# Optimization experiments

Hardware: AMD Instinct MI355X
Metric: run time of the kernel (lower is better)

## Reference

```python
import jax, jax.numpy as jnp
import numpy as np

OUT, IN = 11008, 4096  # LLaMA-7B FFN up-projection


def _unpack(packed, shape):
    """Unpack 2-bit fields (4 ternary values per byte, stored as q+1 in {0,1,2})."""
    shifts = jnp.arange(4, dtype=packed.dtype) * 2
    vals = (packed[:, None] >> shifts) & 3            # [n_bytes, 4]
    n = shape[0] * shape[1]
    q = vals.reshape(-1)[:n].astype(jnp.float32) - 1.0  # back to {-1,0,1}
    return q.reshape(shape)


def _pack(q):
    """Pack ternary int values {-1,0,1} -> 2-bit fields, 4 per byte."""
    flat = (q + 1).reshape(-1)
    pad = (-flat.shape[0]) % 4
    flat = jnp.pad(flat, (0, pad))
    groups = flat.reshape(-1, 4)
    weights = (jnp.int32(1) << (jnp.arange(4, dtype=jnp.int32) * 2))
    return jnp.sum(groups * weights, axis=1).astype(jnp.int32)


def setup_inputs() -> dict:
    key = jax.random.key(0)
    kx, kw = jax.random.split(key)
    x = jax.random.normal(kx, (4, 2048, IN), dtype=jnp.float32)
    # build a realistic weight, then absmean-quantize it (per output row)
    W = jax.random.normal(kw, (OUT, IN), dtype=jnp.float32) * 0.02
    weight_scale = jnp.mean(jnp.abs(W), axis=1, keepdims=True)  # [OUT, 1]
    q = jnp.clip(jnp.round(W / weight_scale), -1.0, 1.0).astype(jnp.int32)
    packed_weight = _pack(q)  # [OUT*IN/4] int32 bytes
    return {"x": x, "packed_weight": packed_weight, "weight_scale": weight_scale}


def reference(x, packed_weight, weight_scale):
    # unpack ternary weights, dequantize via per-row scale, dense GEMM
    W = _unpack(packed_weight, (OUT, IN)) * weight_scale  # [OUT, IN] fp32
    return jnp.einsum('bsi,oi->bso', x, W)
```

## Files before the change

kernel.cpp:

```cpp
#include <hip/hip_runtime.h>
#include <hip/hip_bf16.h>


#define M_DIM 8192
#define N_DIM 11008
#define K_DIM 4096
#define BM 128
#define BN 256
#define BK 64
#define KT 64
#define NB_N 43
#define NWG 2752

#define XBF_BYTES ((size_t)M_DIM * K_DIM * 2)
#define BT_BYTES  ((size_t)N_DIM * K_DIM / 4)
#define WS_NEED   (XBF_BYTES + BT_BYTES)

typedef __attribute__((ext_vector_type(8))) short bf16x8;
typedef __attribute__((ext_vector_type(4))) float f32x4;

__device__ inline unsigned int bf16b(float f) {
  union { __hip_bfloat16 h; unsigned short u; } cv;
  cv.h = __float2bfloat16(f);
  return (unsigned int)cv.u;
}

__device__ __forceinline__ void gload_lds16(const void* g, void* l) {
  __builtin_amdgcn_global_load_lds(
      (const __attribute__((address_space(1))) unsigned int*)g,
      (__attribute__((address_space(3))) unsigned int*)l, 16, 0, 0);
}

#define XCVT_BLOCKS 16384
#define PACK_BLOCKS 5504
__global__ __launch_bounds__(256)
void xcvt_kernel(const float* __restrict__ X, unsigned short* __restrict__ Xbf) {
  const size_t i8 = ((size_t)blockIdx.x * 256 + threadIdx.x) * 8;
  float4 a = *(const float4*)(X + i8);
  float4 c = *(const float4*)(X + i8 + 4);
  uint4 o;
  o.x = bf16b(a.x) | (bf16b(a.y) << 16);
  o.y = bf16b(a.z) | (bf16b(a.w) << 16);
  o.z = bf16b(c.x) | (bf16b(c.y) << 16);
  o.w = bf16b(c.z) | (bf16b(c.w) << 16);
  *(uint4*)(Xbf + i8) = o;
}

__global__ __launch_bounds__(256)
void btight_kernel(const int* __restrict__ PW, unsigned char* __restrict__ Bt) {
  const size_t i8 = ((size_t)blockIdx.x * 256 + threadIdx.x) * 8;
  int4 p = *(const int4*)(PW + i8);
  int4 q = *(const int4*)(PW + i8 + 4);
  uint2 o;
  o.x = (unsigned)(p.x & 255) | ((unsigned)(p.y & 255) << 8) |
        ((unsigned)(p.z & 255) << 16) | ((unsigned)(p.w & 255) << 24);
  o.y = (unsigned)(q.x & 255) | ((unsigned)(q.y & 255) << 8) |
        ((unsigned)(q.z & 255) << 16) | ((unsigned)(q.w & 255) << 24);
  *(uint2*)(Bt + i8) = o;
}

__global__ __launch_bounds__(256, 2)
void qlin_p4_kernel(const unsigned short* __restrict__ Xbf,
                    const unsigned char* __restrict__ Bt,
                    const float* __restrict__ SC, float* __restrict__ OUT) {
  __shared__ unsigned short As[3][BM * BK];
  __shared__ unsigned char  Bs[3][BN * 16];

  const int tid = threadIdx.x;
  const int lane = tid & 63;
  const int w = tid >> 6;

  const int wg = blockIdx.x;
  const int swz = (wg & 7) * (NWG / 8) + (wg >> 3);
  const int bm = swz / NB_N;
  const int bn = swz - bm * NB_N;

  const int l3 = lane >> 3;
  const char* ab0 = (const char*)Xbf +
      (size_t)(bm * BM + w * 32 + l3) * (K_DIM * 2) + ((lane & 7) ^ l3) * 16;
  const char* bb = (const char*)Bt + (size_t)(bn * BN + w * 64 + lane) * (K_DIM / 4);

#define STAGE(IDX, KT_) do {                                           \
    unsigned short* ad_ = &As[IDX][w * 2048];                          \
    unsigned char* bd_ = &Bs[IDX][w * 1024];                           \
    gload_lds16(ab0 + (KT_)*128,           ad_);                       \
    gload_lds16(ab0 + (KT_)*128 + 65536,   ad_ + 512);                 \
    gload_lds16(ab0 + (KT_)*128 + 131072,  ad_ + 1024);                \
    gload_lds16(ab0 + (KT_)*128 + 196608,  ad_ + 1536);                \
    gload_lds16(bb  + (KT_)*16,            bd_);                       \
  } while (0)

  f32x4 acc[8][4];
#pragma unroll
  for (int i = 0; i < 8; ++i)
#pragma unroll
    for (int j = 0; j < 4; ++j) acc[i][j] = (f32x4){0.f, 0.f, 0.f, 0.f};

  const int l4 = lane >> 4;
  const int axor = lane & 7;
  const int arow = (lane & 15) * 128;
  const int hb = l4 >> 1;
  const unsigned hoff = (unsigned)(l4 & 1) * 16;
  const int rbase = (w * 64 + (lane & 15)) * 16 + hb * 4;

  bf16x8 af[4];
  bf16x8 bfr[4];
  unsigned d4[4];

#define DSA(CB, KK, H) do {                                                    \
    const char* asb_ = (const char*)&As[CB][0];                                \
    _Pragma("unroll")                                                          \
    for (int m = 0; m < 4; ++m)                                                \
      af[m] = *(const bf16x8*)(asb_ + ((H) * 4 + m) * 2048 + arow +            \
                               ((((KK) * 4 + l4) ^ axor) << 4));               \
  } while (0)

#define DSB(CB, KK) do {                                                       \
    const unsigned char* bsb_ = &Bs[CB][0];                                    \
    _Pragma("unroll")                                                          \
    for (int n = 0; n < 4; ++n)                                                \
      d4[n] = *(const unsigned*)(bsb_ + rbase + n * 256 + (KK) * 8);           \
  } while (0)

#define UNPACK() do {                                                          \
    _Pragma("unroll")                                                          \
    for (int n = 0; n < 4; ++n) {                                              \
      const unsigned w16 = (d4[n] >> hoff) & 0xFFFFu;                          \
      const unsigned u = w16 | (w16 << 14);                                    \
      union { uint4 s; bf16x8 v; } t;                                          \
      t.s.x = ((u << 14) & 0xC000C000u) + 0x40004000u;                         \
      t.s.y = ((u << 10) & 0xC000C000u) + 0x40004000u;                         \
      t.s.z = ((u << 6)  & 0xC000C000u) + 0x40004000u;                         \
      t.s.w = ((u << 2)  & 0xC000C000u) + 0x40004000u;                         \
      bfr[n] = t.v;                                                            \
    }                                                                          \
  } while (0)

#define MFMA16(H) do {                                                         \
    _Pragma("unroll")                                                          \
    for (int m = 0; m < 4; ++m)                                                \
      _Pragma("unroll")                                                        \
      for (int n = 0; n < 4; ++n)                                              \
        acc[(H) * 4 + m][n] = __builtin_amdgcn_mfma_f32_16x16x32_bf16(         \
            af[m], bfr[n], acc[(H) * 4 + m][n], 0, 0, 0);                      \
  } while (0)

#define BAR() __builtin_amdgcn_s_barrier()
#define LGKM0() asm volatile("s_waitcnt lgkmcnt(0)" ::: "memory")
#define PRIO(P) __builtin_amdgcn_s_setprio(P)

  STAGE(0, 0);
  STAGE(1, 1);
  asm volatile("s_waitcnt vmcnt(5)" ::: "memory");
  BAR();

  int cb = 0, sb = 2;
  for (int kt = 0; kt < KT; ++kt) {
    const bool more = (kt + 2 < KT);
    DSA(cb, 0, 0);
    DSB(cb, 0);
    if (more) STAGE(sb, kt + 2);
    BAR(); LGKM0(); PRIO(1);
    UNPACK();
    MFMA16(0);
    PRIO(0); BAR();
    DSA(cb, 0, 1);
    BAR(); LGKM0(); PRIO(1);
    MFMA16(1);
    PRIO(0); BAR();
    DSA(cb, 1, 0);
    DSB(cb, 1);
    BAR(); LGKM0(); PRIO(1);
    UNPACK();
    MFMA16(0);
    PRIO(0); BAR();
    DSA(cb, 1, 1);
    if (more) { asm volatile("s_waitcnt vmcnt(5)" ::: "memory"); }
    else      { asm volatile("s_waitcnt vmcnt(0)" ::: "memory"); }
    BAR(); LGKM0(); PRIO(1);
    MFMA16(1);
    PRIO(0); BAR();
    cb = (cb == 2) ? 0 : cb + 1;
    sb = (sb == 2) ? 0 : sb + 1;
  }
#undef STAGE
#undef DSA
#undef DSB
#undef UNPACK
#undef MFMA16

  const int gc0 = bn * BN + w * 64 + (lane & 15);
  const int gr0 = bm * BM + (l4 << 2);
  float sc[4];
#pragma unroll
  for (int n = 0; n < 4; ++n) sc[n] = -0.5f * SC[gc0 + n * 16];
#pragma unroll
  for (int m = 0; m < 8; ++m)
#pragma unroll
    for (int n = 0; n < 4; ++n)
#pragma unroll
      for (int r = 0; r < 4; ++r)
        OUT[(size_t)(gr0 + m * 16 + r) * N_DIM + gc0 + n * 16] = acc[m][n][r] * sc[n];
}

#define BSTRIDE 20
__global__ __launch_bounds__(256, 2)
void qlin_fused_kernel(const float* __restrict__ X, const int* __restrict__ PW,
                       const float* __restrict__ SC, float* __restrict__ OUT) {
  __shared__ unsigned short Asf[128 * 64];
  __shared__ unsigned char Bp[256 * BSTRIDE];

  const int tid = threadIdx.x;
  const int wg = blockIdx.x;
  const int swz = (wg & 7) * (NWG / 8) + (wg >> 3);
  const int bm = swz / NB_N;
  const int bn = swz - bm * NB_N;

  const int lane = tid & 63;
  const int wave = tid >> 6;
  const int wr = wave >> 1;
  const int wc = wave & 1;

  const int arow = tid >> 3;
  const int ac8  = tid & 7;
  const float* xptr = X + (size_t)(bm * 128 + arow) * K_DIM + ac8 * 8;
  const unsigned int aswz = ((unsigned)arow & 7u) << 4;

  const int bc  = tid & 3;
  const int br0 = tid >> 2;
  const int* pwptr = PW + (size_t)(bn * 256 + br0) * (K_DIM / 4) + bc * 4;
  const int bwoff = (bc & 1) * 8 + (bc >> 1) * 2;

  f32x4 acc[4][8];
#pragma unroll
  for (int i = 0; i < 4; ++i)
#pragma unroll
    for (int j = 0; j < 8; ++j) acc[i][j] = (f32x4){0.f, 0.f, 0.f, 0.f};

  float4 av[4][2];
  int4 bv[4];
#pragma unroll
  for (int j = 0; j < 4; ++j) {
    av[j][0] = *(const float4*)(xptr + (size_t)(32 * j) * K_DIM);
    av[j][1] = *(const float4*)(xptr + (size_t)(32 * j) * K_DIM + 4);
  }
#pragma unroll
  for (int j = 0; j < 4; ++j)
    bv[j] = *(const int4*)(pwptr + (size_t)(64 * j) * (K_DIM / 4));

  for (int kt = 0; kt < KT; ++kt) {
    __syncthreads();
#pragma unroll
    for (int j = 0; j < 4; ++j) {
      uint4 wv;
      wv.x = bf16b(av[j][0].x) | (bf16b(av[j][0].y) << 16);
      wv.y = bf16b(av[j][0].z) | (bf16b(av[j][0].w) << 16);
      wv.z = bf16b(av[j][1].x) | (bf16b(av[j][1].y) << 16);
      wv.w = bf16b(av[j][1].z) | (bf16b(av[j][1].w) << 16);
      *(uint4*)((char*)Asf + (arow + 32 * j) * 128 + (((unsigned)ac8 * 16u) ^ aswz)) = wv;
    }
#pragma unroll
    for (int j = 0; j < 4; ++j) {
      const unsigned int ulo = ((unsigned)bv[j].x & 255u) | (((unsigned)bv[j].y & 255u) << 8);
      const unsigned int uhi = ((unsigned)bv[j].z & 255u) | (((unsigned)bv[j].w & 255u) << 8);
      unsigned char* dst = Bp + (br0 + 64 * j) * BSTRIDE + bwoff;
      *(unsigned short*)(dst)     = (unsigned short)ulo;
      *(unsigned short*)(dst + 4) = (unsigned short)uhi;
    }
    __syncthreads();

    if (kt + 1 < KT) {
#pragma unroll
      for (int j = 0; j < 4; ++j) {
        av[j][0] = *(const float4*)(xptr + (kt + 1) * BK + (size_t)(32 * j) * K_DIM);
        av[j][1] = *(const float4*)(xptr + (kt + 1) * BK + (size_t)(32 * j) * K_DIM + 4);
      }
#pragma unroll
      for (int j = 0; j < 4; ++j)
        bv[j] = *(const int4*)(pwptr + (kt + 1) * 16 + (size_t)(64 * j) * (K_DIM / 4));
    }

    const int bh = lane >> 4;
    const int bcol0 = wc * 128 + (lane & 15);
    unsigned int d[8];
#pragma unroll
    for (int n = 0; n < 8; ++n)
      d[n] = *(const unsigned int*)(Bp + (bcol0 + n * 16) * BSTRIDE + bh * 4);

    const unsigned int rswz = ((unsigned)lane & 7u) << 4;
#pragma unroll
    for (int kk = 0; kk < 2; ++kk) {
      bf16x8 af[4];
      const unsigned int coff = (((unsigned)(kk * 4 + (lane >> 4))) * 16u) ^ rswz;
#pragma unroll
      for (int m = 0; m < 4; ++m)
        af[m] = *(const bf16x8*)((const char*)Asf + (wr * 64 + m * 16 + (lane & 15)) * 128 + coff);
#pragma unroll
      for (int n = 0; n < 8; ++n) {
        const unsigned int w16 = kk ? (d[n] >> 16) : (d[n] & 0xFFFFu);
        const unsigned int u = w16 | (w16 << 14);
        union { uint4 s; bf16x8 v; } bfr;
        bfr.s.x = ((u << 14) & 0xC000C000u) + 0x40004000u;
        bfr.s.y = ((u << 10) & 0xC000C000u) + 0x40004000u;
        bfr.s.z = ((u << 6)  & 0xC000C000u) + 0x40004000u;
        bfr.s.w = ((u << 2)  & 0xC000C000u) + 0x40004000u;
#pragma unroll
        for (int m = 0; m < 4; ++m)
          acc[m][n] = __builtin_amdgcn_mfma_f32_16x16x32_bf16(af[m], bfr.v, acc[m][n], 0, 0, 0);
      }
    }
  }

  const int gc0 = bn * 256 + wc * 128 + (lane & 15);
  const int gr0 = bm * 128 + wr * 64 + ((lane >> 4) << 2);
  float sc[8];
#pragma unroll
  for (int n = 0; n < 8; ++n) sc[n] = -0.5f * SC[gc0 + n * 16];
#pragma unroll
  for (int m = 0; m < 4; ++m)
#pragma unroll
    for (int n = 0; n < 8; ++n)
#pragma unroll
      for (int r = 0; r < 4; ++r)
        OUT[(size_t)(gr0 + m * 16 + r) * N_DIM + gc0 + n * 16] = acc[m][n][r] * sc[n];
}

extern "C" void kernel_launch(void* const* d_in, const int* in_sizes, int n_in,
                              void* d_out, int out_size, void* d_ws, size_t ws_size,
                              hipStream_t stream) {
  const float* x  = (const float*)d_in[0];
  const int*   pw = (const int*)d_in[1];
  const float* sc = (const float*)d_in[2];
  float* out = (float*)d_out;
  (void)in_sizes; (void)n_in; (void)out_size;

  if (ws_size >= WS_NEED) {
    unsigned short* xbf = (unsigned short*)d_ws;
    unsigned char* bt = (unsigned char*)d_ws + XBF_BYTES;
    xcvt_kernel<<<dim3(XCVT_BLOCKS), dim3(256), 0, stream>>>(x, xbf);
    btight_kernel<<<dim3(PACK_BLOCKS), dim3(256), 0, stream>>>(pw, bt);
    qlin_p4_kernel<<<dim3(NWG), dim3(256), 0, stream>>>(xbf, bt, sc, out);
  } else {
    qlin_fused_kernel<<<dim3(NWG), dim3(256), 0, stream>>>(x, pw, sc, out);
  }
}
```

Before: 700.1 us.

## Double M tile to 256 with 8-wave workgroups sharing ternary B tile

```diff
diff --git a/kernel.cpp b/kernel.cpp
--- a/kernel.cpp
+++ b/kernel.cpp
@@ -5,12 +5,12 @@
 #define M_DIM 8192
 #define N_DIM 11008
 #define K_DIM 4096
-#define BM 128
+#define BM 256
 #define BN 256
 #define BK 64
 #define KT 64
 #define NB_N 43
-#define NWG 2752
+#define NWG 1376
 
 #define XBF_BYTES ((size_t)M_DIM * K_DIM * 2)
 #define BT_BYTES  ((size_t)N_DIM * K_DIM / 4)
@@ -59,16 +59,19 @@
   *(uint2*)(Bt + i8) = o;
 }
 
-__global__ __launch_bounds__(256, 2)
-void qlin_p4_kernel(const unsigned short* __restrict__ Xbf,
+__global__ __launch_bounds__(512, 2)
+void qlin_w8_kernel(const unsigned short* __restrict__ Xbf,
                     const unsigned char* __restrict__ Bt,
                     const float* __restrict__ SC, float* __restrict__ OUT) {
   __shared__ unsigned short As[3][BM * BK];
   __shared__ unsigned char  Bs[3][BN * 16];
+  __shared__ unsigned char  Bdummy[4 * 1024];
 
   const int tid = threadIdx.x;
   const int lane = tid & 63;
   const int w = tid >> 6;
+  const int wm = w >> 2;
+  const int wn = w & 3;
 
   const int wg = blockIdx.x;
   const int swz = (wg & 7) * (NWG / 8) + (wg >> 3);
@@ -78,16 +81,19 @@
   const int l3 = lane >> 3;
   const char* ab0 = (const char*)Xbf +
       (size_t)(bm * BM + w * 32 + l3) * (K_DIM * 2) + ((lane & 7) ^ l3) * 16;
-  const char* bb = (const char*)Bt + (size_t)(bn * BN + w * 64 + lane) * (K_DIM / 4);
+  const char* bb = (const char*)Bt +
+      (size_t)(bn * BN + (w & 3) * 64 + lane) * (K_DIM / 4);
+  unsigned char* bdst[3];
+  if (w < 4) { bdst[0] = &Bs[0][w * 1024]; bdst[1] = &Bs[1][w * 1024]; bdst[2] = &Bs[2][w * 1024]; }
+  else       { bdst[0] = bdst[1] = bdst[2] = &Bdummy[(w - 4) * 1024]; }
 
 #define STAGE(IDX, KT_) do {                                           \
     unsigned short* ad_ = &As[IDX][w * 2048];                          \
-    unsigned char* bd_ = &Bs[IDX][w * 1024];                           \
     gload_lds16(ab0 + (KT_)*128,           ad_);                       \
     gload_lds16(ab0 + (KT_)*128 + 65536,   ad_ + 512);                 \
     gload_lds16(ab0 + (KT_)*128 + 131072,  ad_ + 1024);                \
     gload_lds16(ab0 + (KT_)*128 + 196608,  ad_ + 1536);                \
-    gload_lds16(bb  + (KT_)*16,            bd_);                       \
+    gload_lds16(bb  + (KT_)*16,            bdst[IDX]);                 \
   } while (0)
 
   f32x4 acc[8][4];
@@ -98,10 +104,10 @@
 
   const int l4 = lane >> 4;
   const int axor = lane & 7;
-  const int arow = (lane & 15) * 128;
+  const int arowb = (wm * 128 + (lane & 15)) * 128;
   const int hb = l4 >> 1;
   const unsigned hoff = (unsigned)(l4 & 1) * 16;
-  const int rbase = (w * 64 + (lane & 15)) * 16 + hb * 4;
+  const int rbase = (wn * 64 + (lane & 15)) * 16 + hb * 4;
 
   bf16x8 af[4];
   bf16x8 bfr[4];
@@ -111,7 +117,7 @@
     const char* asb_ = (const char*)&As[CB][0];                                \
     _Pragma("unroll")                                                          \
     for (int m = 0; m < 4; ++m)                                                \
-      af[m] = *(const bf16x8*)(asb_ + ((H) * 4 + m) * 2048 + arow +            \
+      af[m] = *(const bf16x8*)(asb_ + arowb + ((H) * 4 + m) * 2048 +           \
                                ((((KK) * 4 + l4) ^ axor) << 4));               \
   } while (0)
 
@@ -156,10 +162,9 @@
 
   int cb = 0, sb = 2;
   for (int kt = 0; kt < KT; ++kt) {
-    const bool more = (kt + 2 < KT);
     DSA(cb, 0, 0);
     DSB(cb, 0);
-    if (more) STAGE(sb, kt + 2);
+    if (kt + 2 < KT) STAGE(sb, kt + 2);
     BAR(); LGKM0(); PRIO(1);
     UNPACK();
     MFMA16(0);
@@ -175,8 +180,8 @@
     MFMA16(0);
     PRIO(0); BAR();
     DSA(cb, 1, 1);
-    if (more) { asm volatile("s_waitcnt vmcnt(5)" ::: "memory"); }
-    else      { asm volatile("s_waitcnt vmcnt(0)" ::: "memory"); }
+    if (kt < KT - 2) { asm volatile("s_waitcnt vmcnt(5)" ::: "memory"); }
+    else             { asm volatile("s_waitcnt vmcnt(0)" ::: "memory"); }
     BAR(); LGKM0(); PRIO(1);
     MFMA16(1);
     PRIO(0); BAR();
@@ -189,8 +194,8 @@
 #undef UNPACK
 #undef MFMA16
 
-  const int gc0 = bn * BN + w * 64 + (lane & 15);
-  const int gr0 = bm * BM + (l4 << 2);
+  const int gc0 = bn * BN + wn * 64 + (lane & 15);
+  const int gr0 = bm * BM + wm * 128 + (l4 << 2);
   float sc[4];
 #pragma unroll
   for (int n = 0; n < 4; ++n) sc[n] = -0.5f * SC[gc0 + n * 16];
@@ -203,6 +208,7 @@
         OUT[(size_t)(gr0 + m * 16 + r) * N_DIM + gc0 + n * 16] = acc[m][n][r] * sc[n];
 }
 
+#define FB_NWG 2752
 #define BSTRIDE 20
 __global__ __launch_bounds__(256, 2)
 void qlin_fused_kernel(const float* __restrict__ X, const int* __restrict__ PW,
@@ -212,9 +218,9 @@
 
   const int tid = threadIdx.x;
   const int wg = blockIdx.x;
-  const int swz = (wg & 7) * (NWG / 8) + (wg >> 3);
-  const int bm = swz / NB_N;
-  const int bn = swz - bm * NB_N;
+  const int swz = (wg & 7) * (FB_NWG / 8) + (wg >> 3);
+  const int bm = swz / 43;
+  const int bn = swz - bm * 43;
 
   const int lane = tid & 63;
   const int wave = tid >> 6;
@@ -248,7 +254,7 @@
   for (int j = 0; j < 4; ++j)
     bv[j] = *(const int4*)(pwptr + (size_t)(64 * j) * (K_DIM / 4));
 
-  for (int kt = 0; kt < KT; ++kt) {
+  for (int kt = 0; kt < 64; ++kt) {
     __syncthreads();
 #pragma unroll
     for (int j = 0; j < 4; ++j) {
@@ -269,11 +275,11 @@
     }
     __syncthreads();
 
-    if (kt + 1 < KT) {
+    if (kt + 1 < 64) {
 #pragma unroll
       for (int j = 0; j < 4; ++j) {
-        av[j][0] = *(const float4*)(xptr + (kt + 1) * BK + (size_t)(32 * j) * K_DIM);
-        av[j][1] = *(const float4*)(xptr + (kt + 1) * BK + (size_t)(32 * j) * K_DIM + 4);
+        av[j][0] = *(const float4*)(xptr + (kt + 1) * 64 + (size_t)(32 * j) * K_DIM);
+        av[j][1] = *(const float4*)(xptr + (kt + 1) * 64 + (size_t)(32 * j) * K_DIM + 4);
       }
 #pragma unroll
       for (int j = 0; j < 4; ++j)
@@ -339,8 +345,8 @@
     unsigned char* bt = (unsigned char*)d_ws + XBF_BYTES;
     xcvt_kernel<<<dim3(XCVT_BLOCKS), dim3(256), 0, stream>>>(x, xbf);
     btight_kernel<<<dim3(PACK_BLOCKS), dim3(256), 0, stream>>>(pw, bt);
-    qlin_p4_kernel<<<dim3(NWG), dim3(256), 0, stream>>>(xbf, bt, sc, out);
+    qlin_w8_kernel<<<dim3(NWG), dim3(512), 0, stream>>>(xbf, bt, sc, out);
   } else {
-    qlin_fused_kernel<<<dim3(NWG), dim3(256), 0, stream>>>(x, pw, sc, out);
+    qlin_fused_kernel<<<dim3(FB_NWG), dim3(256), 0, stream>>>(x, pw, sc, out);
   }
 }
```

After: 915.5 us. +30.8%, slower.
